# Optimization experiments

Hardware: AMD Instinct MI355X
Metric: run time of the kernel (lower is better)

Reference implementation:

```python
import jax, jax.numpy as jnp
import numpy as np

N = 40000      # nodes
E = 640000     # edges
D = 128        # input_dim == hidden_dim
G = 64         # graphs in batch


def _mk_linear(key, din, dout):
    kw, kb = jax.random.split(key)
    w = jax.random.normal(kw, (din, dout), jnp.float32) / np.sqrt(din)
    b = jax.random.normal(kb, (dout,), jnp.float32) * 0.01
    return w, b


def setup_inputs() -> dict:
    key = jax.random.key(0)
    ks = jax.random.split(key, 12)
    x = jax.random.normal(ks[0], (N, D), jnp.float32)
    edge_attr = jax.random.normal(ks[1], (E, D), jnp.float32)
    edge_index = jax.random.randint(ks[2], (2, E), 0, N, jnp.int32)
    batch = jnp.sort(jax.random.randint(ks[3], (N,), 0, G, jnp.int32))
    inp = {"x": x, "edge_attr": edge_attr, "edge_index": edge_index, "batch": batch}
    # 4 GINE layers, each with a 2-layer MLP (Linear-ReLU-Linear)
    for i in range(4):
        w1, b1 = _mk_linear(ks[4 + 2 * i], D, D)
        w2, b2 = _mk_linear(ks[5 + 2 * i], D, D)
        inp[f"w{i+1}_1"] = w1
        inp[f"b{i+1}_1"] = b1
        inp[f"w{i+1}_2"] = w2
        inp[f"b{i+1}_2"] = b2
    return inp


def _gine_layer(x, src, dst, edge_attr, w1, b1, w2, b2):
    # message: ReLU(x_src + edge_attr), scatter-sum into dst (PyG GINEConv, eps=0)
    msg = jax.nn.relu(x[src] + edge_attr)                      # [E, D]
    agg = jax.ops.segment_sum(msg, dst, num_segments=N)       # [N, D]
    h = x + agg                                                # (1+eps)*x + agg, eps=0
    h = jnp.maximum(h @ w1 + b1, 0.0) @ w2 + b2                # 2-layer MLP
    return h


def reference(x, edge_attr, edge_index, batch,
              w1_1, b1_1, w1_2, b1_2,
              w2_1, b2_1, w2_2, b2_2,
              w3_1, b3_1, w3_2, b3_2,
              w4_1, b4_1, w4_2, b4_2):
    src, dst = edge_index[0], edge_index[1]
    h = x
    params = [(w1_1, b1_1, w1_2, b1_2), (w2_1, b2_1, w2_2, b2_2),
              (w3_1, b3_1, w3_2, b3_2), (w4_1, b4_1, w4_2, b4_2)]
    for (w1, b1, w2, b2) in params:
        h = jax.nn.relu(_gine_layer(h, src, dst, edge_attr, w1, b1, w2, b2))
    # global mean pool over graphs
    sums = jax.ops.segment_sum(h, batch, num_segments=G)                 # [G, D]
    cnts = jax.ops.segment_sum(jnp.ones((N,), h.dtype), batch, num_segments=G)
    return sums / jnp.maximum(cnts, 1.0)[:, None]
```

## Files before the change

### kernel.cpp

```cpp
#include <hip/hip_runtime.h>

#define NN 40000
#define NE 640000
#define DD 128
#define NG 64

typedef float vf4 __attribute__((ext_vector_type(4)));
typedef unsigned short us4 __attribute__((ext_vector_type(4)));
typedef unsigned short us8 __attribute__((ext_vector_type(8)));
typedef short bf16x8 __attribute__((ext_vector_type(8)));
typedef float f32x4 __attribute__((ext_vector_type(4)));

__device__ inline unsigned short f2bf(float f) {
    unsigned int u = __float_as_uint(f);
    return (unsigned short)((u + 0x7fffu + ((u >> 16) & 1u)) >> 16);
}
__device__ inline float bf2f(unsigned short s) {
    return __uint_as_float((unsigned int)s << 16);
}

#define PRE_CVT_BLKS  2500
#define PRE_W_BLKS    512
#define PRE_H_BLKS    2500
#define PRE_BLOCKS    (PRE_CVT_BLKS + PRE_W_BLKS + PRE_H_BLKS)

template <int USE_BF>
__global__ __launch_bounds__(256) void preamble_k(
    const float* __restrict__ x, unsigned short* __restrict__ hB,
    const float* __restrict__ m0, const float* __restrict__ m1,
    const float* __restrict__ m2, const float* __restrict__ m3,
    const float* __restrict__ m4, const float* __restrict__ m5,
    const float* __restrict__ m6, const float* __restrict__ m7,
    unsigned short* __restrict__ whi, unsigned short* __restrict__ wlo,
    const int* __restrict__ dst, int* __restrict__ cnt)
{
    const int bid = blockIdx.x;
    if (bid < PRE_CVT_BLKS) {
        if (!USE_BF) return;
        size_t i = ((size_t)bid * 256 + threadIdx.x) * 8;
        vf4 a = __builtin_nontemporal_load((const vf4*)(x + i));
        vf4 b = __builtin_nontemporal_load((const vf4*)(x + i + 4));
        us4 o0 = {f2bf(a.x), f2bf(a.y), f2bf(a.z), f2bf(a.w)};
        us4 o1 = {f2bf(b.x), f2bf(b.y), f2bf(b.z), f2bf(b.w)};
        *(us4*)(hB + i) = o0;
        *(us4*)(hB + i + 4) = o1;
    } else if (bid < PRE_CVT_BLKS + PRE_W_BLKS) {
        const float* ms[8] = {m0, m1, m2, m3, m4, m5, m6, m7};
        int b = bid - PRE_CVT_BLKS;
        int mat = b >> 6;
        int idx = (b & 63) * 256 + threadIdx.x;
        float v = ms[mat][idx];
        int k = idx >> 7, n = idx & 127;
        unsigned short h = f2bf(v);
        size_t o = ((size_t)mat << 14) + (size_t)n * DD + k;
        whi[o] = h;
        wlo[o] = f2bf(v - bf2f(h));
    } else {
        int e = (bid - PRE_CVT_BLKS - PRE_W_BLKS) * 256 + threadIdx.x;
        if (e < NE) atomicAdd(&cnt[dst[e]], 1);
    }
}

__global__ __launch_bounds__(1024) void scan_k(const int* __restrict__ cnt,
                                               int* __restrict__ row_ptr,
                                               int* __restrict__ cursor)
{
    __shared__ int sm[1024];
    int t = threadIdx.x;
    int base = t * 40;
    int4 buf[10];
    if (base + 40 <= NN) {
#pragma unroll
        for (int i = 0; i < 10; ++i) buf[i] = ((const int4*)(cnt + base))[i];
    } else {
#pragma unroll
        for (int i = 0; i < 10; ++i) {
            int idx = base + i * 4;
            int4 v = make_int4(0, 0, 0, 0);
            if (idx + 0 < NN) v.x = cnt[idx + 0];
            if (idx + 1 < NN) v.y = cnt[idx + 1];
            if (idx + 2 < NN) v.z = cnt[idx + 2];
            if (idx + 3 < NN) v.w = cnt[idx + 3];
            buf[i] = v;
        }
    }
    int s = 0;
#pragma unroll
    for (int i = 0; i < 10; ++i) s += buf[i].x + buf[i].y + buf[i].z + buf[i].w;
    sm[t] = s;
    __syncthreads();
    for (int off = 1; off < 1024; off <<= 1) {
        int x = (t >= off) ? sm[t - off] : 0;
        __syncthreads();
        sm[t] += x;
        __syncthreads();
    }
    int run = sm[t] - s;
#pragma unroll
    for (int i = 0; i < 10; ++i) {
        int idx = base + i * 4;
        if (idx + 0 < NN) { row_ptr[idx + 0] = run; cursor[idx + 0] = run; run += buf[i].x; }
        if (idx + 1 < NN) { row_ptr[idx + 1] = run; cursor[idx + 1] = run; run += buf[i].y; }
        if (idx + 2 < NN) { row_ptr[idx + 2] = run; cursor[idx + 2] = run; run += buf[i].z; }
        if (idx + 3 < NN) { row_ptr[idx + 3] = run; cursor[idx + 3] = run; run += buf[i].w; }
    }
    if (t == 1023) row_ptr[NN] = run;
}

__global__ __launch_bounds__(256) void fill_k(const int* __restrict__ src,
                                              const int* __restrict__ dst,
                                              int* __restrict__ cursor,
                                              int2* __restrict__ elist)
{
    int e = blockIdx.x * 256 + threadIdx.x;
    if (e < NE) {
        int d = dst[e];
        int pos = atomicAdd(&cursor[d], 1);
        elist[pos] = make_int2(src[e], e);
    }
}

__device__ inline void acc1(float4& acc, const unsigned short* __restrict__ hb,
                            const unsigned short* __restrict__ eb,
                            int s, int id, int lane)
{
    us4 xv = *(const us4*)(hb + (size_t)s * DD + lane * 4);
    us4 bv = __builtin_nontemporal_load((const us4*)(eb + (size_t)id * DD + lane * 4));
    acc.x += fmaxf(bf2f(xv.x) + bf2f(bv.x), 0.f);
    acc.y += fmaxf(bf2f(xv.y) + bf2f(bv.y), 0.f);
    acc.z += fmaxf(bf2f(xv.z) + bf2f(bv.z), 0.f);
    acc.w += fmaxf(bf2f(xv.w) + bf2f(bv.w), 0.f);
}

__device__ inline void acc1_cvt(float4& acc, const unsigned short* __restrict__ hb,
                                const float* __restrict__ ea,
                                unsigned short* __restrict__ eb,
                                int s, int id, int lane)
{
    us4 xv = *(const us4*)(hb + (size_t)s * DD + lane * 4);
    vf4 ev = __builtin_nontemporal_load((const vf4*)(ea + (size_t)id * DD + lane * 4));
    us4 bv = {f2bf(ev.x), f2bf(ev.y), f2bf(ev.z), f2bf(ev.w)};
    *(us4*)(eb + (size_t)id * DD + lane * 4) = bv;
    acc.x += fmaxf(bf2f(xv.x) + bf2f(bv.x), 0.f);
    acc.y += fmaxf(bf2f(xv.y) + bf2f(bv.y), 0.f);
    acc.z += fmaxf(bf2f(xv.z) + bf2f(bv.z), 0.f);
    acc.w += fmaxf(bf2f(xv.w) + bf2f(bv.w), 0.f);
}

template <int L0>
__global__ __launch_bounds__(256) void gather_bf(
    const unsigned short* __restrict__ hb, const unsigned short* __restrict__ eb_r,
    const float* __restrict__ ea, unsigned short* __restrict__ eb_w,
    const int* __restrict__ row_ptr, const int2* __restrict__ elist,
    float* __restrict__ agg)
{
    int grp = blockIdx.x * 8 + (threadIdx.x >> 5);
    int lane = threadIdx.x & 31;
    if (grp >= NN) return;
    int beg = row_ptr[grp], end = row_ptr[grp + 1];

    float4 a0 = make_float4(0.f, 0.f, 0.f, 0.f);
    float4 a1 = make_float4(0.f, 0.f, 0.f, 0.f);
    float4 a2 = make_float4(0.f, 0.f, 0.f, 0.f);
    float4 a3 = make_float4(0.f, 0.f, 0.f, 0.f);
    int e = beg;
    for (; e + 4 <= end; e += 4) {
        int2 p0 = elist[e];
        int2 p1 = elist[e + 1];
        int2 p2 = elist[e + 2];
        int2 p3 = elist[e + 3];
        if (L0) {
            acc1_cvt(a0, hb, ea, eb_w, p0.x, p0.y, lane);
            acc1_cvt(a1, hb, ea, eb_w, p1.x, p1.y, lane);
            acc1_cvt(a2, hb, ea, eb_w, p2.x, p2.y, lane);
            acc1_cvt(a3, hb, ea, eb_w, p3.x, p3.y, lane);
        } else {
            acc1(a0, hb, eb_r, p0.x, p0.y, lane);
            acc1(a1, hb, eb_r, p1.x, p1.y, lane);
            acc1(a2, hb, eb_r, p2.x, p2.y, lane);
            acc1(a3, hb, eb_r, p3.x, p3.y, lane);
        }
    }
    for (; e < end; ++e) {
        int2 p0 = elist[e];
        if (L0) acc1_cvt(a0, hb, ea, eb_w, p0.x, p0.y, lane);
        else    acc1(a0, hb, eb_r, p0.x, p0.y, lane);
    }
    us4 sv = *(const us4*)(hb + (size_t)grp * DD + lane * 4);
    float4 o;
    o.x = bf2f(sv.x) + (a0.x + a1.x) + (a2.x + a3.x);
    o.y = bf2f(sv.y) + (a0.y + a1.y) + (a2.y + a3.y);
    o.z = bf2f(sv.z) + (a0.z + a1.z) + (a2.z + a3.z);
    o.w = bf2f(sv.w) + (a0.w + a1.w) + (a2.w + a3.w);
    *(float4*)(agg + (size_t)grp * DD + lane * 4) = o;
}

__device__ inline void acc1f(float4& acc, const float* __restrict__ h,
                             const float* __restrict__ ea,
                             int s, int id, int lane)
{
    const float4 xv = *(const float4*)(h + (size_t)s * DD + lane * 4);
    vf4 ev = __builtin_nontemporal_load((const vf4*)(ea + (size_t)id * DD + lane * 4));
    acc.x += fmaxf(xv.x + ev.x, 0.f);
    acc.y += fmaxf(xv.y + ev.y, 0.f);
    acc.z += fmaxf(xv.z + ev.z, 0.f);
    acc.w += fmaxf(xv.w + ev.w, 0.f);
}

__global__ __launch_bounds__(256) void gather_f32(
    const float* __restrict__ h, const float* __restrict__ ea,
    const int* __restrict__ row_ptr, const int2* __restrict__ elist,
    float* __restrict__ agg)
{
    int grp = blockIdx.x * 8 + (threadIdx.x >> 5);
    int lane = threadIdx.x & 31;
    if (grp >= NN) return;
    int beg = row_ptr[grp], end = row_ptr[grp + 1];

    float4 a0 = make_float4(0.f, 0.f, 0.f, 0.f);
    float4 a1 = make_float4(0.f, 0.f, 0.f, 0.f);
    float4 a2 = make_float4(0.f, 0.f, 0.f, 0.f);
    float4 a3 = make_float4(0.f, 0.f, 0.f, 0.f);
    int e = beg;
    for (; e + 4 <= end; e += 4) {
        int2 p0 = elist[e];
        int2 p1 = elist[e + 1];
        int2 p2 = elist[e + 2];
        int2 p3 = elist[e + 3];
        acc1f(a0, h, ea, p0.x, p0.y, lane);
        acc1f(a1, h, ea, p1.x, p1.y, lane);
        acc1f(a2, h, ea, p2.x, p2.y, lane);
        acc1f(a3, h, ea, p3.x, p3.y, lane);
    }
    for (; e < end; ++e) {
        int2 p0 = elist[e];
        acc1f(a0, h, ea, p0.x, p0.y, lane);
    }
    const float4 sv = *(const float4*)(h + (size_t)grp * DD + lane * 4);
    float4 o;
    o.x = sv.x + (a0.x + a1.x) + (a2.x + a3.x);
    o.y = sv.y + (a0.y + a1.y) + (a2.y + a3.y);
    o.z = sv.z + (a0.z + a1.z) + (a2.z + a3.z);
    o.w = sv.w + (a0.w + a1.w) + (a2.w + a3.w);
    *(float4*)(agg + (size_t)grp * DD + lane * 4) = o;
}

template <int OUT>
__global__ __launch_bounds__(256, 2) void mlp_fused(
    const float* __restrict__ A,
    const unsigned short* __restrict__ W1h, const unsigned short* __restrict__ W1l,
    const float* __restrict__ b1v,
    const unsigned short* __restrict__ W2h, const unsigned short* __restrict__ W2l,
    const float* __restrict__ b2v,
    float* C, unsigned short* Cb)
{
    __shared__ __align__(16) char lds[64 * 1024];
    char* lAh = lds;
    char* lAl = lds + 16 * 1024;
    char* lBh = lds + 32 * 1024;
    char* lBl = lds + 48 * 1024;

    const int tid = threadIdx.x;
    const int m0 = blockIdx.x * 64;

    const int wc  = tid >> 2;
    const int wk0 = (tid & 3) * 32;
    const int wbase = wc * 256 + wk0 * 2;
    const int wsw = (wc & 7) << 4;
    auto stageW = [&](const unsigned short* Wh_, const unsigned short* Wl_,
                      int col0) {
        const unsigned short* sh = Wh_ + (size_t)(col0 + wc) * DD + wk0;
        const unsigned short* sl = Wl_ + (size_t)(col0 + wc) * DD + wk0;
#pragma unroll
        for (int i = 0; i < 4; ++i) {
            const int off = (wbase + i * 16) ^ wsw;
            *(us8*)(lBh + off) = *(const us8*)(sh + i * 8);
            *(us8*)(lBl + off) = *(const us8*)(sl + i * 8);
        }
    };

    {
        const int row = tid >> 2;
        const int c0 = (tid & 3) * 32;
        const float* srcp = A + (size_t)(m0 + row) * DD + c0;
        const int base = row * 256 + c0 * 2;
        const int sw = (row & 7) << 4;
#pragma unroll
        for (int i = 0; i < 4; ++i) {
            float4 v0 = *(const float4*)(srcp + i * 8);
            float4 v1 = *(const float4*)(srcp + i * 8 + 4);
            float f[8] = {v0.x, v0.y, v0.z, v0.w, v1.x, v1.y, v1.z, v1.w};
            us8 hv, lv;
#pragma unroll
            for (int j = 0; j < 8; ++j) {
                unsigned short hb = f2bf(f[j]);
                hv[j] = hb;
                lv[j] = f2bf(f[j] - bf2f(hb));
            }
            const int off = (base + i * 16) ^ sw;
            *(us8*)(lAh + off) = hv;
            *(us8*)(lAl + off) = lv;
        }
    }
    stageW(W1h, W1l, 0);
    __syncthreads();

    const int lane = tid & 63;
    const int wid = tid >> 6;
    const int lr = lane & 15;
    const int kg = lane >> 4;
    const int swr = (lr & 7) << 4;

    bf16x8 ah[4], al[4];
    auto loadA = [&]() {
#pragma unroll
        for (int ks = 0; ks < 4; ++ks) {
            const int off = ((wid * 16 + lr) * 256 + ks * 64 + kg * 16) ^ swr;
            ah[ks] = *(const bf16x8*)(lAh + off);
            al[ks] = *(const bf16x8*)(lAl + off);
        }
    };
    f32x4 acc[8];
    auto mfma_half = [&](int ab) {
#pragma unroll
        for (int nfl = 0; nfl < 4; ++nfl) {
#pragma unroll
            for (int ks = 0; ks < 4; ++ks) {
                const int off = ((nfl * 16 + lr) * 256 + ks * 64 + kg * 16) ^ swr;
                bf16x8 bh = *(const bf16x8*)(lBh + off);
                bf16x8 bl = *(const bf16x8*)(lBl + off);
                acc[ab + nfl] = __builtin_amdgcn_mfma_f32_16x16x32_bf16(ah[ks], bh, acc[ab + nfl], 0, 0, 0);
                acc[ab + nfl] = __builtin_amdgcn_mfma_f32_16x16x32_bf16(ah[ks], bl, acc[ab + nfl], 0, 0, 0);
                acc[ab + nfl] = __builtin_amdgcn_mfma_f32_16x16x32_bf16(al[ks], bh, acc[ab + nfl], 0, 0, 0);
            }
        }
    };

    loadA();
#pragma unroll
    for (int nf = 0; nf < 8; ++nf) acc[nf] = (f32x4){0.f, 0.f, 0.f, 0.f};
    mfma_half(0);
    __syncthreads();
    stageW(W1h, W1l, 64);
    __syncthreads();
    mfma_half(4);
    __syncthreads();

#pragma unroll
    for (int nf = 0; nf < 8; ++nf) {
        const int col = nf * 16 + lr;
        const float b = b1v[col];
#pragma unroll
        for (int r = 0; r < 4; ++r) {
            float u = fmaxf(acc[nf][r] + b, 0.0f);
            const int lrow = wid * 16 + kg * 4 + r;
            const int off = (lrow * 256 + col * 2) ^ ((lrow & 7) << 4);
            unsigned short hb = f2bf(u);
            *(unsigned short*)(lAh + off) = hb;
            *(unsigned short*)(lAl + off) = f2bf(u - bf2f(hb));
        }
    }
    stageW(W2h, W2l, 0);
    __syncthreads();

    loadA();
#pragma unroll
    for (int nf = 0; nf < 8; ++nf) acc[nf] = (f32x4){0.f, 0.f, 0.f, 0.f};
    mfma_half(0);
    __syncthreads();
    stageW(W2h, W2l, 64);
    __syncthreads();
    mfma_half(4);

#pragma unroll
    for (int nf = 0; nf < 8; ++nf) {
        const int col = nf * 16 + lr;
        const float b = b2v[col];
        float v[4];
#pragma unroll
        for (int r = 0; r < 4; ++r) v[r] = fmaxf(acc[nf][r] + b, 0.0f);
        const size_t rbase = (size_t)(m0 + wid * 16 + kg * 4) * DD + col;
        if (OUT & 1) {
#pragma unroll
            for (int r = 0; r < 4; ++r) C[rbase + (size_t)r * DD] = v[r];
        }
        if (OUT & 2) {
#pragma unroll
            for (int r = 0; r < 4; ++r) Cb[rbase + (size_t)r * DD] = f2bf(v[r]);
        }
    }
}

__device__ inline void pool_flush(float* __restrict__ out, int g, int lane,
                                  const float4& acc)
{
    float* o = out + (size_t)g * DD + lane * 4;
    unsafeAtomicAdd(o + 0, acc.x);
    unsafeAtomicAdd(o + 1, acc.y);
    unsafeAtomicAdd(o + 2, acc.z);
    unsafeAtomicAdd(o + 3, acc.w);
}

__global__ __launch_bounds__(256) void pool_k(
    const float* __restrict__ h, const int* __restrict__ batch,
    float* __restrict__ out, int* __restrict__ cnt)
{
    int tid = blockIdx.x * 256 + threadIdx.x;
    int grp = tid >> 5;
    int lane = tid & 31;
    int n0 = grp * 16;
    if (n0 >= NN) return;
    int nend = min(n0 + 16, NN);

    float4 acc = make_float4(0.f, 0.f, 0.f, 0.f);
    int gprev = batch[n0];
    int crun = 0;
    for (int n = n0; n < nend; ++n) {
        int g = batch[n];
        if (g != gprev) {
            pool_flush(out, gprev, lane, acc);
            if (lane == 0) atomicAdd(cnt + gprev, crun);
            acc = make_float4(0.f, 0.f, 0.f, 0.f);
            crun = 0;
            gprev = g;
        }
        float4 v = *(const float4*)(h + (size_t)n * DD + lane * 4);
        acc.x += v.x; acc.y += v.y; acc.z += v.z; acc.w += v.w;
        ++crun;
    }
    pool_flush(out, gprev, lane, acc);
    if (lane == 0) atomicAdd(cnt + gprev, crun);
}

__global__ __launch_bounds__(256) void pool_div_k(float* __restrict__ out,
                                                  const int* __restrict__ cnt)
{
    int tid = blockIdx.x * 256 + threadIdx.x;
    if (tid >= NG * DD) return;
    int g = tid / DD;
    float c = fmaxf((float)cnt[g], 1.0f);
    out[tid] = out[tid] / c;
}

extern "C" void kernel_launch(void* const* d_in, const int* in_sizes, int n_in,
                              void* d_out, int out_size, void* d_ws, size_t ws_size,
                              hipStream_t stream)
{
    const float* x     = (const float*)d_in[0];
    const float* ea    = (const float*)d_in[1];
    const int*   ei    = (const int*)d_in[2];
    const int*   batch = (const int*)d_in[3];
    const float* w1[4], * b1[4], * w2[4], * b2[4];
    for (int l = 0; l < 4; ++l) {
        w1[l] = (const float*)d_in[4 + 4 * l];
        b1[l] = (const float*)d_in[5 + 4 * l];
        w2[l] = (const float*)d_in[6 + 4 * l];
        b2[l] = (const float*)d_in[7 + 4 * l];
    }

    const int* srcp = ei;
    const int* dstp = ei + NE;

    char* ws = (char*)d_ws;
    const size_t hbytes = (size_t)NN * DD * sizeof(float);
    float* agg = (float*)ws;
    float* hA  = (float*)(ws + hbytes);
    char*  p   = ws + 2 * hbytes;
    int*  cnt_node = (int*)p;           p += ((NN * 4 + 255) & ~255);
    int*  row_ptr  = (int*)p;           p += (((NN + 1) * 4 + 255) & ~255);
    int*  cursor   = (int*)p;           p += ((NN * 4 + 255) & ~255);
    int2* elist    = (int2*)p;          p += (((size_t)NE * 8 + 255) & ~255);
    int*  cntG     = (int*)p;           p += 256;
    unsigned short* wt_hi = (unsigned short*)p;  p += (size_t)8 * 16384 * 2;
    unsigned short* wt_lo = (unsigned short*)p;  p += (size_t)8 * 16384 * 2;
    unsigned short* hB = (unsigned short*)p;     p += (size_t)NN * DD * 2;
    unsigned short* ea_bf = (unsigned short*)p;
    const size_t need_bf = (size_t)(p - ws) + (size_t)NE * DD * 2;
    const bool use_bf = (ws_size >= need_bf);

    const int eblocks     = (NE + 255) / 256;
    const int gblocks     = (NN + 7) / 8;
    const int gemm_blocks = NN / 64;
    const int pool_blocks = ((NN / 16) * 32 + 255) / 256;

    hipMemsetAsync(cnt_node, 0, NN * sizeof(int), stream);
    if (use_bf)
        preamble_k<1><<<PRE_BLOCKS, 256, 0, stream>>>(
            x, hB, w1[0], w2[0], w1[1], w2[1], w1[2], w2[2], w1[3], w2[3],
            wt_hi, wt_lo, dstp, cnt_node);
    else
        preamble_k<0><<<PRE_BLOCKS, 256, 0, stream>>>(
            x, nullptr, w1[0], w2[0], w1[1], w2[1], w1[2], w2[2], w1[3], w2[3],
            wt_hi, wt_lo, dstp, cnt_node);
    scan_k<<<1, 1024, 0, stream>>>(cnt_node, row_ptr, cursor);
    fill_k<<<eblocks, 256, 0, stream>>>(srcp, dstp, cursor, elist);

    if (use_bf) {
        for (int l = 0; l < 4; ++l) {
            if (l == 0)
                gather_bf<1><<<gblocks, 256, 0, stream>>>(hB, nullptr, ea, ea_bf,
                                                          row_ptr, elist, agg);
            else
                gather_bf<0><<<gblocks, 256, 0, stream>>>(hB, ea_bf, nullptr, nullptr,
                                                          row_ptr, elist, agg);
            const unsigned short* h1  = wt_hi + ((size_t)(2 * l) << 14);
            const unsigned short* lo1 = wt_lo + ((size_t)(2 * l) << 14);
            const unsigned short* h2  = wt_hi + ((size_t)(2 * l + 1) << 14);
            const unsigned short* lo2 = wt_lo + ((size_t)(2 * l + 1) << 14);
            if (l < 3)
                mlp_fused<2><<<gemm_blocks, 256, 0, stream>>>(
                    agg, h1, lo1, b1[l], h2, lo2, b2[l], nullptr, hB);
            else
                mlp_fused<1><<<gemm_blocks, 256, 0, stream>>>(
                    agg, h1, lo1, b1[l], h2, lo2, b2[l], hA, nullptr);
        }
    } else {
        const float* hcur = x;
        for (int l = 0; l < 4; ++l) {
            gather_f32<<<gblocks, 256, 0, stream>>>(hcur, ea, row_ptr, elist, agg);
            const unsigned short* h1  = wt_hi + ((size_t)(2 * l) << 14);
            const unsigned short* lo1 = wt_lo + ((size_t)(2 * l) << 14);
            const unsigned short* h2  = wt_hi + ((size_t)(2 * l + 1) << 14);
            const unsigned short* lo2 = wt_lo + ((size_t)(2 * l + 1) << 14);
            mlp_fused<1><<<gemm_blocks, 256, 0, stream>>>(
                agg, h1, lo1, b1[l], h2, lo2, b2[l], hA, nullptr);
            hcur = hA;
        }
    }

    hipMemsetAsync(d_out, 0, (size_t)NG * DD * sizeof(float), stream);
    hipMemsetAsync(cntG, 0, NG * sizeof(int), stream);
    pool_k<<<pool_blocks, 256, 0, stream>>>(hA, batch, (float*)d_out, cntG);
    pool_div_k<<<(NG * DD + 255) / 256, 256, 0, stream>>>((float*)d_out, cntG);
}
```

Baseline: 884.2 us.

## Fuse edge gather, MLP and mean-pool into one kernel per GINE layer

Each layer's gather-aggregate is now computed directly into shared memory as bf16 hi/lo split A-tiles, and the two-layer MFMA MLP runs on them in the same kernel. This removes the fp32 agg round trip through global memory and one launch per layer. The last layer also does the graph pooling in-kernel with atomics. Edge attributes are rewritten in CSR order and a separate source-index array is added, so later layers stream ea_bf sequentially. Costs include ping-pong bf16 h buffers, per-block serial gathering of 64 nodes before the MFMA phase, and possibly lower occupancy from 64KB of LDS.

```diff
diff --git a/kernel.cpp b/kernel.cpp
--- a/kernel.cpp
+++ b/kernel.cpp
@@ -22,7 +22,8 @@
 #define PRE_CVT_BLKS  2500
 #define PRE_W_BLKS    512
 #define PRE_H_BLKS    2500
-#define PRE_BLOCKS    (PRE_CVT_BLKS + PRE_W_BLKS + PRE_H_BLKS)
+#define PRE_B_BLKS    157
+#define PRE_BLOCKS    (PRE_CVT_BLKS + PRE_W_BLKS + PRE_H_BLKS + PRE_B_BLKS)
 
 template <int USE_BF>
 __global__ __launch_bounds__(256) void preamble_k(
@@ -32,7 +33,8 @@
     const float* __restrict__ m4, const float* __restrict__ m5,
     const float* __restrict__ m6, const float* __restrict__ m7,
     unsigned short* __restrict__ whi, unsigned short* __restrict__ wlo,
-    const int* __restrict__ dst, int* __restrict__ cnt)
+    const int* __restrict__ dst, int* __restrict__ cnt,
+    const int* __restrict__ batch, int* __restrict__ cntG)
 {
     const int bid = blockIdx.x;
     if (bid < PRE_CVT_BLKS) {
@@ -55,9 +57,13 @@
         size_t o = ((size_t)mat << 14) + (size_t)n * DD + k;
         whi[o] = h;
         wlo[o] = f2bf(v - bf2f(h));
-    } else {
+    } else if (bid < PRE_CVT_BLKS + PRE_W_BLKS + PRE_H_BLKS) {
         int e = (bid - PRE_CVT_BLKS - PRE_W_BLKS) * 256 + threadIdx.x;
         if (e < NE) atomicAdd(&cnt[dst[e]], 1);
+    } else {
+        if (!USE_BF) return;
+        int n = (bid - PRE_CVT_BLKS - PRE_W_BLKS - PRE_H_BLKS) * 256 + threadIdx.x;
+        if (n < NN) atomicAdd(&cntG[batch[n]], 1);
     }
 }
 
@@ -110,89 +116,221 @@
 __global__ __launch_bounds__(256) void fill_k(const int* __restrict__ src,
                                               const int* __restrict__ dst,
                                               int* __restrict__ cursor,
-                                              int2* __restrict__ elist)
+                                              int2* __restrict__ elist,
+                                              int* __restrict__ srcA)
 {
     int e = blockIdx.x * 256 + threadIdx.x;
     if (e < NE) {
         int d = dst[e];
+        int s = src[e];
         int pos = atomicAdd(&cursor[d], 1);
-        elist[pos] = make_int2(src[e], e);
-    }
-}
-
-__device__ inline void acc1(float4& acc, const unsigned short* __restrict__ hb,
-                            const unsigned short* __restrict__ eb,
-                            int s, int id, int lane)
-{
-    us4 xv = *(const us4*)(hb + (size_t)s * DD + lane * 4);
-    us4 bv = __builtin_nontemporal_load((const us4*)(eb + (size_t)id * DD + lane * 4));
-    acc.x += fmaxf(bf2f(xv.x) + bf2f(bv.x), 0.f);
-    acc.y += fmaxf(bf2f(xv.y) + bf2f(bv.y), 0.f);
-    acc.z += fmaxf(bf2f(xv.z) + bf2f(bv.z), 0.f);
-    acc.w += fmaxf(bf2f(xv.w) + bf2f(bv.w), 0.f);
-}
-
-__device__ inline void acc1_cvt(float4& acc, const unsigned short* __restrict__ hb,
-                                const float* __restrict__ ea,
-                                unsigned short* __restrict__ eb,
-                                int s, int id, int lane)
-{
-    us4 xv = *(const us4*)(hb + (size_t)s * DD + lane * 4);
-    vf4 ev = __builtin_nontemporal_load((const vf4*)(ea + (size_t)id * DD + lane * 4));
-    us4 bv = {f2bf(ev.x), f2bf(ev.y), f2bf(ev.z), f2bf(ev.w)};
-    *(us4*)(eb + (size_t)id * DD + lane * 4) = bv;
-    acc.x += fmaxf(bf2f(xv.x) + bf2f(bv.x), 0.f);
-    acc.y += fmaxf(bf2f(xv.y) + bf2f(bv.y), 0.f);
-    acc.z += fmaxf(bf2f(xv.z) + bf2f(bv.z), 0.f);
-    acc.w += fmaxf(bf2f(xv.w) + bf2f(bv.w), 0.f);
-}
-
-template <int L0>
-__global__ __launch_bounds__(256) void gather_bf(
-    const unsigned short* __restrict__ hb, const unsigned short* __restrict__ eb_r,
-    const float* __restrict__ ea, unsigned short* __restrict__ eb_w,
-    const int* __restrict__ row_ptr, const int2* __restrict__ elist,
-    float* __restrict__ agg)
-{
-    int grp = blockIdx.x * 8 + (threadIdx.x >> 5);
-    int lane = threadIdx.x & 31;
-    if (grp >= NN) return;
-    int beg = row_ptr[grp], end = row_ptr[grp + 1];
-
-    float4 a0 = make_float4(0.f, 0.f, 0.f, 0.f);
-    float4 a1 = make_float4(0.f, 0.f, 0.f, 0.f);
-    float4 a2 = make_float4(0.f, 0.f, 0.f, 0.f);
-    float4 a3 = make_float4(0.f, 0.f, 0.f, 0.f);
-    int e = beg;
-    for (; e + 4 <= end; e += 4) {
-        int2 p0 = elist[e];
-        int2 p1 = elist[e + 1];
-        int2 p2 = elist[e + 2];
-        int2 p3 = elist[e + 3];
-        if (L0) {
-            acc1_cvt(a0, hb, ea, eb_w, p0.x, p0.y, lane);
-            acc1_cvt(a1, hb, ea, eb_w, p1.x, p1.y, lane);
-            acc1_cvt(a2, hb, ea, eb_w, p2.x, p2.y, lane);
-            acc1_cvt(a3, hb, ea, eb_w, p3.x, p3.y, lane);
-        } else {
-            acc1(a0, hb, eb_r, p0.x, p0.y, lane);
-            acc1(a1, hb, eb_r, p1.x, p1.y, lane);
-            acc1(a2, hb, eb_r, p2.x, p2.y, lane);
-            acc1(a3, hb, eb_r, p3.x, p3.y, lane);
-        }
-    }
-    for (; e < end; ++e) {
-        int2 p0 = elist[e];
-        if (L0) acc1_cvt(a0, hb, ea, eb_w, p0.x, p0.y, lane);
-        else    acc1(a0, hb, eb_r, p0.x, p0.y, lane);
-    }
-    us4 sv = *(const us4*)(hb + (size_t)grp * DD + lane * 4);
-    float4 o;
-    o.x = bf2f(sv.x) + (a0.x + a1.x) + (a2.x + a3.x);
-    o.y = bf2f(sv.y) + (a0.y + a1.y) + (a2.y + a3.y);
-    o.z = bf2f(sv.z) + (a0.z + a1.z) + (a2.z + a3.z);
-    o.w = bf2f(sv.w) + (a0.w + a1.w) + (a2.w + a3.w);
-    *(float4*)(agg + (size_t)grp * DD + lane * 4) = o;
+        elist[pos] = make_int2(s, e);
+        srcA[pos] = s;
+    }
+}
+
+template <int L0, int POOL>
+__global__ __launch_bounds__(256, 2) void layer_fused(
+    const unsigned short* __restrict__ hb_in,
+    const float* __restrict__ ea, unsigned short* __restrict__ ea_bf,
+    const int2* __restrict__ elist, const int* __restrict__ srcA,
+    const int* __restrict__ row_ptr,
+    const unsigned short* __restrict__ W1h, const unsigned short* __restrict__ W1l,
+    const float* __restrict__ b1v,
+    const unsigned short* __restrict__ W2h, const unsigned short* __restrict__ W2l,
+    const float* __restrict__ b2v,
+    unsigned short* __restrict__ hb_out,
+    float* __restrict__ outp, const int* __restrict__ batch)
+{
+    __shared__ __align__(16) char lds[64 * 1024];
+    __shared__ int sbatch[64];
+    char* lAh = lds;
+    char* lAl = lds + 16 * 1024;
+    char* lBh = lds + 32 * 1024;
+    char* lBl = lds + 48 * 1024;
+
+    const int tid = threadIdx.x;
+    const int m0 = blockIdx.x * 64;
+
+    {
+        const int g = tid >> 5;
+        const int lane = tid & 31;
+#pragma unroll 1
+        for (int i = 0; i < 8; ++i) {
+            const int nl = g * 8 + i;
+            const int node = m0 + nl;
+            const int beg = row_ptr[node], end = row_ptr[node + 1];
+            float4 a0 = make_float4(0.f, 0.f, 0.f, 0.f);
+            float4 a1 = make_float4(0.f, 0.f, 0.f, 0.f);
+            float4 a2 = make_float4(0.f, 0.f, 0.f, 0.f);
+            float4 a3 = make_float4(0.f, 0.f, 0.f, 0.f);
+            auto edge = [&](float4& acc, int pos) {
+                us4 xv, bv;
+                if (L0) {
+                    int2 pr = elist[pos];
+                    xv = *(const us4*)(hb_in + (size_t)pr.x * DD + lane * 4);
+                    vf4 ev = __builtin_nontemporal_load(
+                        (const vf4*)(ea + (size_t)pr.y * DD + lane * 4));
+                    bv = (us4){f2bf(ev.x), f2bf(ev.y), f2bf(ev.z), f2bf(ev.w)};
+                    *(us4*)(ea_bf + (size_t)pos * DD + lane * 4) = bv;
+                } else {
+                    int s = srcA[pos];
+                    xv = *(const us4*)(hb_in + (size_t)s * DD + lane * 4);
+                    bv = __builtin_nontemporal_load(
+                        (const us4*)(ea_bf + (size_t)pos * DD + lane * 4));
+                }
+                acc.x += fmaxf(bf2f(xv.x) + bf2f(bv.x), 0.f);
+                acc.y += fmaxf(bf2f(xv.y) + bf2f(bv.y), 0.f);
+                acc.z += fmaxf(bf2f(xv.z) + bf2f(bv.z), 0.f);
+                acc.w += fmaxf(bf2f(xv.w) + bf2f(bv.w), 0.f);
+            };
+            int pos = beg;
+            for (; pos + 4 <= end; pos += 4) {
+                edge(a0, pos); edge(a1, pos + 1); edge(a2, pos + 2); edge(a3, pos + 3);
+            }
+            for (; pos < end; ++pos) edge(a0, pos);
+            us4 sv = *(const us4*)(hb_in + (size_t)node * DD + lane * 4);
+            float o[4];
+            o[0] = bf2f(sv.x) + (a0.x + a1.x) + (a2.x + a3.x);
+            o[1] = bf2f(sv.y) + (a0.y + a1.y) + (a2.y + a3.y);
+            o[2] = bf2f(sv.z) + (a0.z + a1.z) + (a2.z + a3.z);
+            o[3] = bf2f(sv.w) + (a0.w + a1.w) + (a2.w + a3.w);
+            us4 hv, lv;
+#pragma unroll
+            for (int c = 0; c < 4; ++c) {
+                unsigned short hb = f2bf(o[c]);
+                hv[c] = hb;
+                lv[c] = f2bf(o[c] - bf2f(hb));
+            }
+            const int off = (nl * 256 + lane * 8) ^ ((nl & 7) << 4);
+            *(us4*)(lAh + off) = hv;
+            *(us4*)(lAl + off) = lv;
+        }
+    }
+
+    const int wc  = tid >> 2;
+    const int wk0 = (tid & 3) * 32;
+    const int wbase = wc * 256 + wk0 * 2;
+    const int wsw = (wc & 7) << 4;
+    auto stageW = [&](const unsigned short* Wh_, const unsigned short* Wl_,
+                      int col0) {
+        const unsigned short* sh = Wh_ + (size_t)(col0 + wc) * DD + wk0;
+        const unsigned short* sl = Wl_ + (size_t)(col0 + wc) * DD + wk0;
+#pragma unroll
+        for (int i = 0; i < 4; ++i) {
+            const int off = (wbase + i * 16) ^ wsw;
+            *(us8*)(lBh + off) = *(const us8*)(sh + i * 8);
+            *(us8*)(lBl + off) = *(const us8*)(sl + i * 8);
+        }
+    };
+    stageW(W1h, W1l, 0);
+    __syncthreads();
+
+    const int lane64 = tid & 63;
+    const int wid = tid >> 6;
+    const int lr = lane64 & 15;
+    const int kg = lane64 >> 4;
+    const int swr = (lr & 7) << 4;
+
+    bf16x8 ah[4], al[4];
+    auto loadA = [&]() {
+#pragma unroll
+        for (int ks = 0; ks < 4; ++ks) {
+            const int off = ((wid * 16 + lr) * 256 + ks * 64 + kg * 16) ^ swr;
+            ah[ks] = *(const bf16x8*)(lAh + off);
+            al[ks] = *(const bf16x8*)(lAl + off);
+        }
+    };
+    f32x4 acc[8];
+    auto mfma_half = [&](int ab) {
+#pragma unroll
+        for (int nfl = 0; nfl < 4; ++nfl) {
+#pragma unroll
+            for (int ks = 0; ks < 4; ++ks) {
+                const int off = ((nfl * 16 + lr) * 256 + ks * 64 + kg * 16) ^ swr;
+                bf16x8 bh = *(const bf16x8*)(lBh + off);
+                bf16x8 bl = *(const bf16x8*)(lBl + off);
+                acc[ab + nfl] = __builtin_amdgcn_mfma_f32_16x16x32_bf16(ah[ks], bh, acc[ab + nfl], 0, 0, 0);
+                acc[ab + nfl] = __builtin_amdgcn_mfma_f32_16x16x32_bf16(ah[ks], bl, acc[ab + nfl], 0, 0, 0);
+                acc[ab + nfl] = __builtin_amdgcn_mfma_f32_16x16x32_bf16(al[ks], bh, acc[ab + nfl], 0, 0, 0);
+            }
+        }
+    };
+
+    loadA();
+#pragma unroll
+    for (int nf = 0; nf < 8; ++nf) acc[nf] = (f32x4){0.f, 0.f, 0.f, 0.f};
+    mfma_half(0);
+    __syncthreads();
+    stageW(W1h, W1l, 64);
+    __syncthreads();
+    mfma_half(4);
+    __syncthreads();
+
+#pragma unroll
+    for (int nf = 0; nf < 8; ++nf) {
+        const int col = nf * 16 + lr;
+        const float b = b1v[col];
+#pragma unroll
+        for (int r = 0; r < 4; ++r) {
+            float u = fmaxf(acc[nf][r] + b, 0.0f);
+            const int lrow = wid * 16 + kg * 4 + r;
+            const int off = (lrow * 256 + col * 2) ^ ((lrow & 7) << 4);
+            unsigned short hb = f2bf(u);
+            *(unsigned short*)(lAh + off) = hb;
+            *(unsigned short*)(lAl + off) = f2bf(u - bf2f(hb));
+        }
+    }
+    stageW(W2h, W2l, 0);
+    __syncthreads();
+
+    loadA();
+#pragma unroll
+    for (int nf = 0; nf < 8; ++nf) acc[nf] = (f32x4){0.f, 0.f, 0.f, 0.f};
+    mfma_half(0);
+    __syncthreads();
+    stageW(W2h, W2l, 64);
+    __syncthreads();
+    mfma_half(4);
+
+    if (!POOL) {
+#pragma unroll
+        for (int nf = 0; nf < 8; ++nf) {
+            const int col = nf * 16 + lr;
+            const float b = b2v[col];
+            const size_t rbase = (size_t)(m0 + wid * 16 + kg * 4) * DD + col;
+#pragma unroll
+            for (int r = 0; r < 4; ++r)
+                hb_out[rbase + (size_t)r * DD] = f2bf(fmaxf(acc[nf][r] + b, 0.0f));
+        }
+    } else {
+        float* pstage = (float*)lds;
+        if (tid < 64) sbatch[tid] = batch[m0 + tid];
+#pragma unroll
+        for (int nf = 0; nf < 8; ++nf) {
+            const int col = nf * 16 + lr;
+            const float b = b2v[col];
+            const int row = wid * 16 + kg * 4;
+#pragma unroll
+            for (int r = 0; r < 4; ++r)
+                pstage[(row + r) * DD + col] = fmaxf(acc[nf][r] + b, 0.0f);
+        }
+        __syncthreads();
+        const int col = tid & 127;
+        const int row0 = (tid >> 7) * 32;
+        float run = 0.f;
+        int gprev = sbatch[row0];
+        for (int r = row0; r < row0 + 32; ++r) {
+            int gg = sbatch[r];
+            if (gg != gprev) {
+                unsafeAtomicAdd(outp + (size_t)gprev * DD + col, run);
+                run = 0.f;
+                gprev = gg;
+            }
+            run += pstage[r * DD + col];
+        }
+        unsafeAtomicAdd(outp + (size_t)gprev * DD + col, run);
+    }
 }
 
 __device__ inline void acc1f(float4& acc, const float* __restrict__ h,
@@ -245,14 +383,13 @@
     *(float4*)(agg + (size_t)grp * DD + lane * 4) = o;
 }
 
-template <int OUT>
-__global__ __launch_bounds__(256, 2) void mlp_fused(
+__global__ __launch_bounds__(256, 2) void mlp_f32(
     const float* __restrict__ A,
     const unsigned short* __restrict__ W1h, const unsigned short* __restrict__ W1l,
     const float* __restrict__ b1v,
     const unsigned short* __restrict__ W2h, const unsigned short* __restrict__ W2l,
     const float* __restrict__ b2v,
-    float* C, unsigned short* Cb)
+    float* C)
 {
     __shared__ __align__(16) char lds[64 * 1024];
     char* lAh = lds;
@@ -278,7 +415,6 @@
             *(us8*)(lBl + off) = *(const us8*)(sl + i * 8);
         }
     };
-
     {
         const int row = tid >> 2;
         const int c0 = (tid & 3) * 32;
@@ -305,10 +441,10 @@
     stageW(W1h, W1l, 0);
     __syncthreads();
 
-    const int lane = tid & 63;
+    const int lane64 = tid & 63;
     const int wid = tid >> 6;
-    const int lr = lane & 15;
-    const int kg = lane >> 4;
+    const int lr = lane64 & 15;
+    const int kg = lane64 >> 4;
     const int swr = (lr & 7) << 4;
 
     bf16x8 ah[4], al[4];
@@ -335,7 +471,6 @@
             }
         }
     };
-
     loadA();
 #pragma unroll
     for (int nf = 0; nf < 8; ++nf) acc[nf] = (f32x4){0.f, 0.f, 0.f, 0.f};
@@ -345,7 +480,6 @@
     __syncthreads();
     mfma_half(4);
     __syncthreads();
-
 #pragma unroll
     for (int nf = 0; nf < 8; ++nf) {
         const int col = nf * 16 + lr;
@@ -362,7 +496,6 @@
     }
     stageW(W2h, W2l, 0);
     __syncthreads();
-
     loadA();
 #pragma unroll
     for (int nf = 0; nf < 8; ++nf) acc[nf] = (f32x4){0.f, 0.f, 0.f, 0.f};
@@ -371,23 +504,14 @@
     stageW(W2h, W2l, 64);
     __syncthreads();
     mfma_half(4);
-
 #pragma unroll
     for (int nf = 0; nf < 8; ++nf) {
         const int col = nf * 16 + lr;
         const float b = b2v[col];
-        float v[4];
-#pragma unroll
-        for (int r = 0; r < 4; ++r) v[r] = fmaxf(acc[nf][r] + b, 0.0f);
         const size_t rbase = (size_t)(m0 + wid * 16 + kg * 4) * DD + col;
-        if (OUT & 1) {
-#pragma unroll
-            for (int r = 0; r < 4; ++r) C[rbase + (size_t)r * DD] = v[r];
-        }
-        if (OUT & 2) {
-#pragma unroll
-            for (int r = 0; r < 4; ++r) Cb[rbase + (size_t)r * DD] = f2bf(v[r]);
-        }
+#pragma unroll
+        for (int r = 0; r < 4; ++r)
+            C[rbase + (size_t)r * DD] = fmaxf(acc[nf][r] + b, 0.0f);
     }
 }
 
@@ -470,51 +594,56 @@
     int*  row_ptr  = (int*)p;           p += (((NN + 1) * 4 + 255) & ~255);
     int*  cursor   = (int*)p;           p += ((NN * 4 + 255) & ~255);
     int2* elist    = (int2*)p;          p += (((size_t)NE * 8 + 255) & ~255);
+    int*  srcA     = (int*)p;           p += (((size_t)NE * 4 + 255) & ~255);
     int*  cntG     = (int*)p;           p += 256;
     unsigned short* wt_hi = (unsigned short*)p;  p += (size_t)8 * 16384 * 2;
     unsigned short* wt_lo = (unsigned short*)p;  p += (size_t)8 * 16384 * 2;
-    unsigned short* hB = (unsigned short*)p;     p += (size_t)NN * DD * 2;
+    unsigned short* hB0 = (unsigned short*)p;    p += (size_t)NN * DD * 2;
+    unsigned short* hB1 = (unsigned short*)p;    p += (size_t)NN * DD * 2;
     unsigned short* ea_bf = (unsigned short*)p;
     const size_t need_bf = (size_t)(p - ws) + (size_t)NE * DD * 2;
     const bool use_bf = (ws_size >= need_bf);
 
     const int eblocks     = (NE + 255) / 256;
-    const int gblocks     = (NN + 7) / 8;
     const int gemm_blocks = NN / 64;
     const int pool_blocks = ((NN / 16) * 32 + 255) / 256;
 
     hipMemsetAsync(cnt_node, 0, NN * sizeof(int), stream);
+    hipMemsetAsync(cntG, 0, NG * sizeof(int), stream);
+    hipMemsetAsync(d_out, 0, (size_t)NG * DD * sizeof(float), stream);
     if (use_bf)
         preamble_k<1><<<PRE_BLOCKS, 256, 0, stream>>>(
-            x, hB, w1[0], w2[0], w1[1], w2[1], w1[2], w2[2], w1[3], w2[3],
-            wt_hi, wt_lo, dstp, cnt_node);
+            x, hB0, w1[0], w2[0], w1[1], w2[1], w1[2], w2[2], w1[3], w2[3],
+            wt_hi, wt_lo, dstp, cnt_node, batch, cntG);
     else
         preamble_k<0><<<PRE_BLOCKS, 256, 0, stream>>>(
             x, nullptr, w1[0], w2[0], w1[1], w2[1], w1[2], w2[2], w1[3], w2[3],
-            wt_hi, wt_lo, dstp, cnt_node);
+            wt_hi, wt_lo, dstp, cnt_node, batch, cntG);
     scan_k<<<1, 1024, 0, stream>>>(cnt_node, row_ptr, cursor);
-    fill_k<<<eblocks, 256, 0, stream>>>(srcp, dstp, cursor, elist);
+    fill_k<<<eblocks, 256, 0, stream>>>(srcp, dstp, cursor, elist, srcA);
 
     if (use_bf) {
-        for (int l = 0; l < 4; ++l) {
-            if (l == 0)
-                gather_bf<1><<<gblocks, 256, 0, stream>>>(hB, nullptr, ea, ea_bf,
-                                                          row_ptr, elist, agg);
-            else
-                gather_bf<0><<<gblocks, 256, 0, stream>>>(hB, ea_bf, nullptr, nullptr,
-                                                          row_ptr, elist, agg);
-            const unsigned short* h1  = wt_hi + ((size_t)(2 * l) << 14);
-            const unsigned short* lo1 = wt_lo + ((size_t)(2 * l) << 14);
-            const unsigned short* h2  = wt_hi + ((size_t)(2 * l + 1) << 14);
-            const unsigned short* lo2 = wt_lo + ((size_t)(2 * l + 1) << 14);
-            if (l < 3)
-                mlp_fused<2><<<gemm_blocks, 256, 0, stream>>>(
-                    agg, h1, lo1, b1[l], h2, lo2, b2[l], nullptr, hB);
-            else
-                mlp_fused<1><<<gemm_blocks, 256, 0, stream>>>(
-                    agg, h1, lo1, b1[l], h2, lo2, b2[l], hA, nullptr);
-        }
+        const unsigned short* wh[8];
+        const unsigned short* wl[8];
+        for (int m = 0; m < 8; ++m) {
+            wh[m] = wt_hi + ((size_t)m << 14);
+            wl[m] = wt_lo + ((size_t)m << 14);
+        }
+        layer_fused<1, 0><<<gemm_blocks, 256, 0, stream>>>(
+            hB0, ea, ea_bf, elist, nullptr, row_ptr,
+            wh[0], wl[0], b1[0], wh[1], wl[1], b2[0], hB1, nullptr, nullptr);
+        layer_fused<0, 0><<<gemm_blocks, 256, 0, stream>>>(
+            hB1, nullptr, ea_bf, nullptr, srcA, row_ptr,
+            wh[2], wl[2], b1[1], wh[3], wl[3], b2[1], hB0, nullptr, nullptr);
+        layer_fused<0, 0><<<gemm_blocks, 256, 0, stream>>>(
+            hB0, nullptr, ea_bf, nullptr, srcA, row_ptr,
+            wh[4], wl[4], b1[2], wh[5], wl[5], b2[2], hB1, nullptr, nullptr);
+        layer_fused<0, 1><<<gemm_blocks, 256, 0, stream>>>(
+            hB1, nullptr, ea_bf, nullptr, srcA, row_ptr,
+            wh[6], wl[6], b1[3], wh[7], wl[7], b2[3], nullptr,
+            (float*)d_out, batch);
     } else {
+        const int gblocks = (NN + 7) / 8;
         const float* hcur = x;
         for (int l = 0; l < 4; ++l) {
             gather_f32<<<gblocks, 256, 0, stream>>>(hcur, ea, row_ptr, elist, agg);
@@ -522,14 +651,12 @@
             const unsigned short* lo1 = wt_lo + ((size_t)(2 * l) << 14);
             const unsigned short* h2  = wt_hi + ((size_t)(2 * l + 1) << 14);
             const unsigned short* lo2 = wt_lo + ((size_t)(2 * l + 1) << 14);
-            mlp_fused<1><<<gemm_blocks, 256, 0, stream>>>(
-                agg, h1, lo1, b1[l], h2, lo2, b2[l], hA, nullptr);
+            mlp_f32<<<gemm_blocks, 256, 0, stream>>>(
+                agg, h1, lo1, b1[l], h2, lo2, b2[l], hA);
             hcur = hA;
         }
-    }
-
-    hipMemsetAsync(d_out, 0, (size_t)NG * DD * sizeof(float), stream);
-    hipMemsetAsync(cntG, 0, NG * sizeof(int), stream);
-    pool_k<<<pool_blocks, 256, 0, stream>>>(hA, batch, (float*)d_out, cntG);
+        pool_k<<<pool_blocks, 256, 0, stream>>>(hA, batch, (float*)d_out, cntG);
+    }
+
     pool_div_k<<<(NG * DD + 255) / 256, 256, 0, stream>>>((float*)d_out, cntG);
 }
```

Measured after the change: 1.234 ms. 1.4x slower.

## Fuse mean-pool into last MLP, store edge bf16 in CSR order, bsearch graph counts

Applied to the files above, without the earlier changes.

The final MLP layer now accumulates the pooled sums itself. It stages its output tile in LDS and issues per-graph atomic adds, so the fp32 hidden write and the separate pool kernel go away. The bf16 edge-attribute copy is written in CSR (dst-sorted) order, which makes later gather layers stream it contiguously, and a separate src array replaces the int2 edge list lookup. Graph node counts now come from a binary search over the sorted batch array instead of atomics. These changes add an extra src array and rely on batch being sorted, which the reference guarantees.

```diff
diff --git a/kernel.cpp b/kernel.cpp
--- a/kernel.cpp
+++ b/kernel.cpp
@@ -61,6 +61,23 @@
     }
 }
 
+__global__ __launch_bounds__(128) void bsearch_k(const int* __restrict__ batch,
+                                                 int* __restrict__ cntG)
+{
+    __shared__ int st[NG + 1];
+    int g = threadIdx.x;
+    if (g <= NG) {
+        int lo = 0, hi = NN;
+        while (lo < hi) {
+            int mid = (lo + hi) >> 1;
+            if (batch[mid] < g) lo = mid + 1; else hi = mid;
+        }
+        st[g] = lo;
+    }
+    __syncthreads();
+    if (g < NG) cntG[g] = st[g + 1] - st[g];
+}
+
 __global__ __launch_bounds__(1024) void scan_k(const int* __restrict__ cnt,
                                                int* __restrict__ row_ptr,
                                                int* __restrict__ cursor)
@@ -110,49 +127,25 @@
 __global__ __launch_bounds__(256) void fill_k(const int* __restrict__ src,
                                               const int* __restrict__ dst,
                                               int* __restrict__ cursor,
-                                              int2* __restrict__ elist)
+                                              int2* __restrict__ elist,
+                                              int* __restrict__ srcA)
 {
     int e = blockIdx.x * 256 + threadIdx.x;
     if (e < NE) {
         int d = dst[e];
+        int s = src[e];
         int pos = atomicAdd(&cursor[d], 1);
-        elist[pos] = make_int2(src[e], e);
-    }
-}
-
-__device__ inline void acc1(float4& acc, const unsigned short* __restrict__ hb,
-                            const unsigned short* __restrict__ eb,
-                            int s, int id, int lane)
-{
-    us4 xv = *(const us4*)(hb + (size_t)s * DD + lane * 4);
-    us4 bv = __builtin_nontemporal_load((const us4*)(eb + (size_t)id * DD + lane * 4));
-    acc.x += fmaxf(bf2f(xv.x) + bf2f(bv.x), 0.f);
-    acc.y += fmaxf(bf2f(xv.y) + bf2f(bv.y), 0.f);
-    acc.z += fmaxf(bf2f(xv.z) + bf2f(bv.z), 0.f);
-    acc.w += fmaxf(bf2f(xv.w) + bf2f(bv.w), 0.f);
-}
-
-__device__ inline void acc1_cvt(float4& acc, const unsigned short* __restrict__ hb,
-                                const float* __restrict__ ea,
-                                unsigned short* __restrict__ eb,
-                                int s, int id, int lane)
-{
-    us4 xv = *(const us4*)(hb + (size_t)s * DD + lane * 4);
-    vf4 ev = __builtin_nontemporal_load((const vf4*)(ea + (size_t)id * DD + lane * 4));
-    us4 bv = {f2bf(ev.x), f2bf(ev.y), f2bf(ev.z), f2bf(ev.w)};
-    *(us4*)(eb + (size_t)id * DD + lane * 4) = bv;
-    acc.x += fmaxf(bf2f(xv.x) + bf2f(bv.x), 0.f);
-    acc.y += fmaxf(bf2f(xv.y) + bf2f(bv.y), 0.f);
-    acc.z += fmaxf(bf2f(xv.z) + bf2f(bv.z), 0.f);
-    acc.w += fmaxf(bf2f(xv.w) + bf2f(bv.w), 0.f);
+        elist[pos] = make_int2(s, e);
+        srcA[pos] = s;
+    }
 }
 
 template <int L0>
 __global__ __launch_bounds__(256) void gather_bf(
-    const unsigned short* __restrict__ hb, const unsigned short* __restrict__ eb_r,
-    const float* __restrict__ ea, unsigned short* __restrict__ eb_w,
-    const int* __restrict__ row_ptr, const int2* __restrict__ elist,
-    float* __restrict__ agg)
+    const unsigned short* __restrict__ hb,
+    const float* __restrict__ ea, unsigned short* __restrict__ ea_bf,
+    const int2* __restrict__ elist, const int* __restrict__ srcA,
+    const int* __restrict__ row_ptr, float* __restrict__ agg)
 {
     int grp = blockIdx.x * 8 + (threadIdx.x >> 5);
     int lane = threadIdx.x & 31;
@@ -163,29 +156,32 @@
     float4 a1 = make_float4(0.f, 0.f, 0.f, 0.f);
     float4 a2 = make_float4(0.f, 0.f, 0.f, 0.f);
     float4 a3 = make_float4(0.f, 0.f, 0.f, 0.f);
-    int e = beg;
-    for (; e + 4 <= end; e += 4) {
-        int2 p0 = elist[e];
-        int2 p1 = elist[e + 1];
-        int2 p2 = elist[e + 2];
-        int2 p3 = elist[e + 3];
+    auto edge = [&](float4& acc, int pos) {
+        us4 xv, bv;
         if (L0) {
-            acc1_cvt(a0, hb, ea, eb_w, p0.x, p0.y, lane);
-            acc1_cvt(a1, hb, ea, eb_w, p1.x, p1.y, lane);
-            acc1_cvt(a2, hb, ea, eb_w, p2.x, p2.y, lane);
-            acc1_cvt(a3, hb, ea, eb_w, p3.x, p3.y, lane);
+            int2 pr = elist[pos];
+            xv = *(const us4*)(hb + (size_t)pr.x * DD + lane * 4);
+            vf4 ev = __builtin_nontemporal_load(
+                (const vf4*)(ea + (size_t)pr.y * DD + lane * 4));
+            bv = (us4){f2bf(ev.x), f2bf(ev.y), f2bf(ev.z), f2bf(ev.w)};
+            *(us4*)(ea_bf + (size_t)pos * DD + lane * 4) = bv;
         } else {
-            acc1(a0, hb, eb_r, p0.x, p0.y, lane);
-            acc1(a1, hb, eb_r, p1.x, p1.y, lane);
-            acc1(a2, hb, eb_r, p2.x, p2.y, lane);
-            acc1(a3, hb, eb_r, p3.x, p3.y, lane);
-        }
-    }
-    for (; e < end; ++e) {
-        int2 p0 = elist[e];
-        if (L0) acc1_cvt(a0, hb, ea, eb_w, p0.x, p0.y, lane);
-        else    acc1(a0, hb, eb_r, p0.x, p0.y, lane);
-    }
+            int s = srcA[pos];
+            xv = *(const us4*)(hb + (size_t)s * DD + lane * 4);
+            bv = __builtin_nontemporal_load(
+                (const us4*)(ea_bf + (size_t)pos * DD + lane * 4));
+        }
+        acc.x += fmaxf(bf2f(xv.x) + bf2f(bv.x), 0.f);
+        acc.y += fmaxf(bf2f(xv.y) + bf2f(bv.y), 0.f);
+        acc.z += fmaxf(bf2f(xv.z) + bf2f(bv.z), 0.f);
+        acc.w += fmaxf(bf2f(xv.w) + bf2f(bv.w), 0.f);
+    };
+    int pos = beg;
+    for (; pos + 4 <= end; pos += 4) {
+        edge(a0, pos); edge(a1, pos + 1); edge(a2, pos + 2); edge(a3, pos + 3);
+    }
+    for (; pos < end; ++pos) edge(a0, pos);
+
     us4 sv = *(const us4*)(hb + (size_t)grp * DD + lane * 4);
     float4 o;
     o.x = bf2f(sv.x) + (a0.x + a1.x) + (a2.x + a3.x);
@@ -245,16 +241,18 @@
     *(float4*)(agg + (size_t)grp * DD + lane * 4) = o;
 }
 
-template <int OUT>
+template <int MODE>
 __global__ __launch_bounds__(256, 2) void mlp_fused(
     const float* __restrict__ A,
     const unsigned short* __restrict__ W1h, const unsigned short* __restrict__ W1l,
     const float* __restrict__ b1v,
     const unsigned short* __restrict__ W2h, const unsigned short* __restrict__ W2l,
     const float* __restrict__ b2v,
-    float* C, unsigned short* Cb)
+    float* C, unsigned short* Cb,
+    float* __restrict__ outp, const int* __restrict__ batch)
 {
     __shared__ __align__(16) char lds[64 * 1024];
+    __shared__ int sbatch[64];
     char* lAh = lds;
     char* lAl = lds + 16 * 1024;
     char* lBh = lds + 32 * 1024;
@@ -305,10 +303,10 @@
     stageW(W1h, W1l, 0);
     __syncthreads();
 
-    const int lane = tid & 63;
+    const int lane64 = tid & 63;
     const int wid = tid >> 6;
-    const int lr = lane & 15;
-    const int kg = lane >> 4;
+    const int lr = lane64 & 15;
+    const int kg = lane64 >> 4;
     const int swr = (lr & 7) << 4;
 
     bf16x8 ah[4], al[4];
@@ -372,22 +370,54 @@
     __syncthreads();
     mfma_half(4);
 
-#pragma unroll
-    for (int nf = 0; nf < 8; ++nf) {
-        const int col = nf * 16 + lr;
-        const float b = b2v[col];
-        float v[4];
-#pragma unroll
-        for (int r = 0; r < 4; ++r) v[r] = fmaxf(acc[nf][r] + b, 0.0f);
-        const size_t rbase = (size_t)(m0 + wid * 16 + kg * 4) * DD + col;
-        if (OUT & 1) {
-#pragma unroll
-            for (int r = 0; r < 4; ++r) C[rbase + (size_t)r * DD] = v[r];
-        }
-        if (OUT & 2) {
-#pragma unroll
-            for (int r = 0; r < 4; ++r) Cb[rbase + (size_t)r * DD] = f2bf(v[r]);
-        }
+    if (MODE == 0) {
+#pragma unroll
+        for (int nf = 0; nf < 8; ++nf) {
+            const int col = nf * 16 + lr;
+            const float b = b2v[col];
+            const size_t rbase = (size_t)(m0 + wid * 16 + kg * 4) * DD + col;
+#pragma unroll
+            for (int r = 0; r < 4; ++r)
+                C[rbase + (size_t)r * DD] = fmaxf(acc[nf][r] + b, 0.0f);
+        }
+    } else if (MODE == 1) {
+#pragma unroll
+        for (int nf = 0; nf < 8; ++nf) {
+            const int col = nf * 16 + lr;
+            const float b = b2v[col];
+            const size_t rbase = (size_t)(m0 + wid * 16 + kg * 4) * DD + col;
+#pragma unroll
+            for (int r = 0; r < 4; ++r)
+                Cb[rbase + (size_t)r * DD] = f2bf(fmaxf(acc[nf][r] + b, 0.0f));
+        }
+    } else {
+        float* pstage = (float*)lds;
+        if (tid < 64) sbatch[tid] = batch[m0 + tid];
+        __syncthreads();
+#pragma unroll
+        for (int nf = 0; nf < 8; ++nf) {
+            const int col = nf * 16 + lr;
+            const float b = b2v[col];
+            const int row = wid * 16 + kg * 4;
+#pragma unroll
+            for (int r = 0; r < 4; ++r)
+                pstage[(row + r) * DD + col] = fmaxf(acc[nf][r] + b, 0.0f);
+        }
+        __syncthreads();
+        const int col = tid & 127;
+        const int row0 = (tid >> 7) * 32;
+        float run = 0.f;
+        int gprev = sbatch[row0];
+        for (int r = row0; r < row0 + 32; ++r) {
+            int gg = sbatch[r];
+            if (gg != gprev) {
+                unsafeAtomicAdd(outp + (size_t)gprev * DD + col, run);
+                run = 0.f;
+                gprev = gg;
+            }
+            run += pstage[r * DD + col];
+        }
+        unsafeAtomicAdd(outp + (size_t)gprev * DD + col, run);
     }
 }
 
@@ -403,7 +433,7 @@
 
 __global__ __launch_bounds__(256) void pool_k(
     const float* __restrict__ h, const int* __restrict__ batch,
-    float* __restrict__ out, int* __restrict__ cnt)
+    float* __restrict__ out)
 {
     int tid = blockIdx.x * 256 + threadIdx.x;
     int grp = tid >> 5;
@@ -414,22 +444,17 @@
 
     float4 acc = make_float4(0.f, 0.f, 0.f, 0.f);
     int gprev = batch[n0];
-    int crun = 0;
     for (int n = n0; n < nend; ++n) {
         int g = batch[n];
         if (g != gprev) {
             pool_flush(out, gprev, lane, acc);
-            if (lane == 0) atomicAdd(cnt + gprev, crun);
             acc = make_float4(0.f, 0.f, 0.f, 0.f);
-            crun = 0;
             gprev = g;
         }
         float4 v = *(const float4*)(h + (size_t)n * DD + lane * 4);
         acc.x += v.x; acc.y += v.y; acc.z += v.z; acc.w += v.w;
-        ++crun;
     }
     pool_flush(out, gprev, lane, acc);
-    if (lane == 0) atomicAdd(cnt + gprev, crun);
 }
 
 __global__ __launch_bounds__(256) void pool_div_k(float* __restrict__ out,
@@ -470,6 +495,7 @@
     int*  row_ptr  = (int*)p;           p += (((NN + 1) * 4 + 255) & ~255);
     int*  cursor   = (int*)p;           p += ((NN * 4 + 255) & ~255);
     int2* elist    = (int2*)p;          p += (((size_t)NE * 8 + 255) & ~255);
+    int*  srcA     = (int*)p;           p += (((size_t)NE * 4 + 255) & ~255);
     int*  cntG     = (int*)p;           p += 256;
     unsigned short* wt_hi = (unsigned short*)p;  p += (size_t)8 * 16384 * 2;
     unsigned short* wt_lo = (unsigned short*)p;  p += (size_t)8 * 16384 * 2;
@@ -484,6 +510,7 @@
     const int pool_blocks = ((NN / 16) * 32 + 255) / 256;
 
     hipMemsetAsync(cnt_node, 0, NN * sizeof(int), stream);
+    hipMemsetAsync(d_out, 0, (size_t)NG * DD * sizeof(float), stream);
     if (use_bf)
         preamble_k<1><<<PRE_BLOCKS, 256, 0, stream>>>(
             x, hB, w1[0], w2[0], w1[1], w2[1], w1[2], w2[2], w1[3], w2[3],
@@ -492,27 +519,34 @@
         preamble_k<0><<<PRE_BLOCKS, 256, 0, stream>>>(
             x, nullptr, w1[0], w2[0], w1[1], w2[1], w1[2], w2[2], w1[3], w2[3],
             wt_hi, wt_lo, dstp, cnt_node);
+    bsearch_k<<<1, 128, 0, stream>>>(batch, cntG);
     scan_k<<<1, 1024, 0, stream>>>(cnt_node, row_ptr, cursor);
-    fill_k<<<eblocks, 256, 0, stream>>>(srcp, dstp, cursor, elist);
+    fill_k<<<eblocks, 256, 0, stream>>>(srcp, dstp, cursor, elist, srcA);
 
     if (use_bf) {
+        const unsigned short* wh[8];
+        const unsigned short* wl[8];
+        for (int m = 0; m < 8; ++m) {
+            wh[m] = wt_hi + ((size_t)m << 14);
+            wl[m] = wt_lo + ((size_t)m << 14);
+        }
         for (int l = 0; l < 4; ++l) {
             if (l == 0)
-                gather_bf<1><<<gblocks, 256, 0, stream>>>(hB, nullptr, ea, ea_bf,
-                                                          row_ptr, elist, agg);
+                gather_bf<1><<<gblocks, 256, 0, stream>>>(
+                    hB, ea, ea_bf, elist, nullptr, row_ptr, agg);
             else
-                gather_bf<0><<<gblocks, 256, 0, stream>>>(hB, ea_bf, nullptr, nullptr,
-                                                          row_ptr, elist, agg);
-            const unsigned short* h1  = wt_hi + ((size_t)(2 * l) << 14);
-            const unsigned short* lo1 = wt_lo + ((size_t)(2 * l) << 14);
-            const unsigned short* h2  = wt_hi + ((size_t)(2 * l + 1) << 14);
-            const unsigned short* lo2 = wt_lo + ((size_t)(2 * l + 1) << 14);
+                gather_bf<0><<<gblocks, 256, 0, stream>>>(
+                    hB, nullptr, ea_bf, nullptr, srcA, row_ptr, agg);
             if (l < 3)
+                mlp_fused<1><<<gemm_blocks, 256, 0, stream>>>(
+                    agg, wh[2 * l], wl[2 * l], b1[l],
+                    wh[2 * l + 1], wl[2 * l + 1], b2[l],
+                    nullptr, hB, nullptr, nullptr);
+            else
                 mlp_fused<2><<<gemm_blocks, 256, 0, stream>>>(
-                    agg, h1, lo1, b1[l], h2, lo2, b2[l], nullptr, hB);
-            else
-                mlp_fused<1><<<gemm_blocks, 256, 0, stream>>>(
-                    agg, h1, lo1, b1[l], h2, lo2, b2[l], hA, nullptr);
+                    agg, wh[2 * l], wl[2 * l], b1[l],
+                    wh[2 * l + 1], wl[2 * l + 1], b2[l],
+                    nullptr, nullptr, (float*)d_out, batch);
         }
     } else {
         const float* hcur = x;
@@ -522,14 +556,12 @@
             const unsigned short* lo1 = wt_lo + ((size_t)(2 * l) << 14);
             const unsigned short* h2  = wt_hi + ((size_t)(2 * l + 1) << 14);
             const unsigned short* lo2 = wt_lo + ((size_t)(2 * l + 1) << 14);
-            mlp_fused<1><<<gemm_blocks, 256, 0, stream>>>(
-                agg, h1, lo1, b1[l], h2, lo2, b2[l], hA, nullptr);
+            mlp_fused<0><<<gemm_blocks, 256, 0, stream>>>(
+                agg, h1, lo1, b1[l], h2, lo2, b2[l], hA, nullptr, nullptr, nullptr);
             hcur = hA;
         }
-    }
-
-    hipMemsetAsync(d_out, 0, (size_t)NG * DD * sizeof(float), stream);
-    hipMemsetAsync(cntG, 0, NG * sizeof(int), stream);
-    pool_k<<<pool_blocks, 256, 0, stream>>>(hA, batch, (float*)d_out, cntG);
+        pool_k<<<pool_blocks, 256, 0, stream>>>(hA, batch, (float*)d_out);
+    }
+
     pool_div_k<<<(NG * DD + 255) / 256, 256, 0, stream>>>((float*)d_out, cntG);
 }
```

After: 859.2 us. -2.8%, faster.
